# Kernel tuning notes

Measured on AMD Instinct MI355X. Metric: run time of the kernel, lower is better.

The kernel has to match this reference:

```python
import jax, jax.numpy as jnp
import numpy as np

N_NODES = 50000
N_EDGES = 800000
D_IN = 256
H = 4
D_OUT = 64
NEG_SLOPE = 0.2


def setup_inputs() -> dict:
    key = jax.random.key(0)
    ks = jax.random.split(key, 6)
    feat = jax.random.normal(ks[0], (N_NODES, D_IN), dtype=jnp.float32)
    src = jax.random.randint(ks[1], (N_EDGES,), 0, N_NODES, dtype=jnp.int32)
    dst = jax.random.randint(ks[2], (N_EDGES,), 0, N_NODES, dtype=jnp.int32)
    # Glorot-ish scaled params
    W_src = jax.random.normal(ks[3], (H * D_OUT, D_IN), dtype=jnp.float32) * (1.0 / np.sqrt(D_IN))
    W_dst = jax.random.normal(ks[4], (H * D_OUT, D_IN), dtype=jnp.float32) * (1.0 / np.sqrt(D_IN))
    b_src = jnp.zeros((H * D_OUT,), dtype=jnp.float32)
    b_dst = jnp.zeros((H * D_OUT,), dtype=jnp.float32)
    attn = jax.random.normal(ks[5], (H, D_OUT), dtype=jnp.float32) * (1.0 / np.sqrt(D_OUT))
    return {"feat": feat, "src": src, "dst": dst, "W_src": W_src, "b_src": b_src,
            "W_dst": W_dst, "b_dst": b_dst, "attn": attn}


def reference(feat, src, dst, W_src, b_src, W_dst, b_dst, attn):
    n = feat.shape[0]
    h, d = attn.shape
    # node projections [N, H, D]
    feat_src = (feat @ W_src.T + b_src).reshape(n, h, d)
    feat_dst = (feat @ W_dst.T + b_dst).reshape(n, h, d)
    # edge-wise u + v, LeakyReLU  -> [E, H, D]
    e = jax.nn.leaky_relu(feat_src[src] + feat_dst[dst], negative_slope=NEG_SLOPE)
    # attention logits [E, H]
    score = jnp.einsum('ehd,hd->eh', e, attn)
    # edge softmax over incoming edges per dst node (numerically stable)
    m = jax.ops.segment_max(score, dst, num_segments=n)
    expv = jnp.exp(score - m[dst])
    denom = jax.ops.segment_sum(expv, dst, num_segments=n)
    a = expv / denom[dst]  # [E, H]
    # weighted scatter-sum of source features -> [N, H, D]
    out = jax.ops.segment_sum(feat_src[src] * a[:, :, None], dst, num_segments=n)
    return out
```

## Files before the change

kernel.cpp:

```cpp
#include <hip/hip_runtime.h>
#include <math.h>

#define N_DIN 256
#define N_COUT 256
#define NEG_SLOPE 0.2f
#define L2E 1.44269504f
#define CAP 64

#define LDK2 40

typedef _Float16 f16;
typedef f16 f16x2 __attribute__((ext_vector_type(2)));
typedef f16 f16x4 __attribute__((ext_vector_type(4)));
typedef f16 f16x8 __attribute__((ext_vector_type(8)));
typedef float f32x4 __attribute__((ext_vector_type(4)));
typedef float f32x8 __attribute__((ext_vector_type(8)));

__global__ __launch_bounds__(256) void prep2(
    const float* __restrict__ Wsrc, const float* __restrict__ Wdst,
    f16* __restrict__ wsrc_h, f16* __restrict__ wdst_h,
    int* __restrict__ deg, int n)
{
    const int b = blockIdx.x;
    if (b >= 64) {
        int i = (b - 64) * 256 + threadIdx.x;
        if (i < n) deg[i] = 0;
        return;
    }
    const float* __restrict__ in = (b < 32) ? Wsrc : Wdst;
    f16* __restrict__ out        = (b < 32) ? wsrc_h : wdst_h;
    size_t i = (size_t)(b & 31) * 2048 + (size_t)threadIdx.x * 8;
    float4 v0 = *reinterpret_cast<const float4*>(&in[i]);
    float4 v1 = *reinterpret_cast<const float4*>(&in[i + 4]);
    f16x8 o;
    o[0] = (f16)v0.x; o[1] = (f16)v0.y; o[2] = (f16)v0.z; o[3] = (f16)v0.w;
    o[4] = (f16)v1.x; o[5] = (f16)v1.y; o[6] = (f16)v1.z; o[7] = (f16)v1.w;
    *reinterpret_cast<f16x8*>(&out[i]) = o;
}

__global__ __launch_bounds__(512) void projbucket(
    const float* __restrict__ feat,
    const f16* __restrict__ wsrc_h, const float* __restrict__ bsrc,
    const f16* __restrict__ wdst_h, const float* __restrict__ bdst,
    f16* __restrict__ fsrc_h, f16* __restrict__ fdst_h, int n,
    const int* __restrict__ src, const int* __restrict__ dst,
    int* __restrict__ deg, int* __restrict__ ssrc, int E)
{
    __shared__ f16 Al[2][64 * LDK2];

    const int t = threadIdx.x;
    const int bx = (int)blockIdx.x;

    if (bx % 3 != 0) {
        int bid = bx - bx / 3 - 1;
        int i = bid * 512 + t;
        if (i < E) {
            int d = dst[i];
            int r = atomicAdd(&deg[d], 1);
            if (r < CAP) ssrc[(size_t)d * CAP + r] = src[i];
        }
        return;
    }
    const int gid = bx / 3;

    const int lane = t & 63;
    const int w = t >> 6;
    const int which = w >> 2;
    const int col0 = (w & 3) * 64;
    const f16* __restrict__ Wm     = which ? wdst_h : wsrc_h;
    const float* __restrict__ bias = which ? bdst : bsrc;
    f16* __restrict__ outp         = which ? fdst_h : fsrc_h;
    const int row0 = gid * 64;

    const int lr = lane & 15;
    const int kc = lane >> 4;

    const int arow = t >> 3;
    const int akof = (t & 7) * 4;
    int agrow = row0 + arow;
    if (agrow >= n) agrow = n - 1;
    const float* __restrict__ fbase = &feat[(size_t)agrow * N_DIN + akof];
    const f16* __restrict__ wrow[4] = {
        &Wm[(size_t)(col0 + 0 * 16 + lr) * N_DIN + kc * 8],
        &Wm[(size_t)(col0 + 1 * 16 + lr) * N_DIN + kc * 8],
        &Wm[(size_t)(col0 + 2 * 16 + lr) * N_DIN + kc * 8],
        &Wm[(size_t)(col0 + 3 * 16 + lr) * N_DIN + kc * 8] };

    f32x4 acc[4][4] = {};

    {
        float4 u = *reinterpret_cast<const float4*>(fbase);
        f16x4 av;
        av[0] = (f16)u.x; av[1] = (f16)u.y; av[2] = (f16)u.z; av[3] = (f16)u.w;
        *reinterpret_cast<f16x4*>(&Al[0][arow * LDK2 + akof]) = av;
    }
    f16x8 Wcur[4], Wnxt[4];
    #pragma unroll
    for (int nf = 0; nf < 4; ++nf)
        Wcur[nf] = *reinterpret_cast<const f16x8*>(wrow[nf]);
    __syncthreads();

    int p = 0;
    #pragma unroll
    for (int ks = 0; ks < 8; ++ks) {
        const int k0 = ks * 32;
        float4 nx;
        if (ks < 7) {
            nx = *reinterpret_cast<const float4*>(fbase + k0 + 32);
            #pragma unroll
            for (int nf = 0; nf < 4; ++nf)
                Wnxt[nf] = *reinterpret_cast<const f16x8*>(wrow[nf] + k0 + 32);
        }

        f16x8 afr[4];
        #pragma unroll
        for (int m = 0; m < 4; ++m)
            afr[m] = *reinterpret_cast<const f16x8*>(
                &Al[p][(m * 16 + lr) * LDK2 + kc * 8]);
        #pragma unroll
        for (int nf = 0; nf < 4; ++nf)
            #pragma unroll
            for (int m = 0; m < 4; ++m)
                acc[nf][m] = __builtin_amdgcn_mfma_f32_16x16x32_f16(
                    Wcur[nf], afr[m], acc[nf][m], 0, 0, 0);

        if (ks < 7) {
            f16x4 av;
            av[0] = (f16)nx.x; av[1] = (f16)nx.y; av[2] = (f16)nx.z; av[3] = (f16)nx.w;
            *reinterpret_cast<f16x4*>(&Al[p ^ 1][arow * LDK2 + akof]) = av;
            __syncthreads();
            #pragma unroll
            for (int nf = 0; nf < 4; ++nf) Wcur[nf] = Wnxt[nf];
            p ^= 1;
        }
    }

    #pragma unroll
    for (int nf = 0; nf < 4; ++nf) {
        const int cbase = col0 + nf * 16 + kc * 4;
        const float4 bv = *reinterpret_cast<const float4*>(&bias[cbase]);
        #pragma unroll
        for (int m = 0; m < 4; ++m) {
            const int row = row0 + m * 16 + lr;
            if (row < n) {
                f16x4 o;
                o[0] = (f16)(acc[nf][m][0] + bv.x);
                o[1] = (f16)(acc[nf][m][1] + bv.y);
                o[2] = (f16)(acc[nf][m][2] + bv.z);
                o[3] = (f16)(acc[nf][m][3] + bv.w);
                *reinterpret_cast<f16x4*>(&outp[(size_t)row * N_COUT + cbase]) = o;
            }
        }
    }
}


template<int Q>
__device__ __forceinline__ void gat_batch(
    int e0, int i0m, int i1m,
    const f16* __restrict__ fsrc_h, int cb,
    f16x8 fd, f16x8 aw, f16x8 zz, f16x8 slp,
    float& l, f32x8& acc)
{
    f16x8 fr[Q];
    #pragma unroll
    for (int q = 0; q < Q; ++q) {
        int e = e0 + q;
        int u = __shfl((e < 32) ? i0m : i1m, e & 31, 32);
        fr[q] = *reinterpret_cast<const f16x8*>(&fsrc_h[(size_t)u * N_COUT + cb]);
    }
    float s[Q];
    #pragma unroll
    for (int q = 0; q < Q; ++q) {
        f16x8 x = fr[q] + fd;
        f16x8 e = slp * __builtin_elementwise_min(x, zz)
                + __builtin_elementwise_max(x, zz);
        f16x2 e0v = { e[0], e[1] }, e1v = { e[2], e[3] };
        f16x2 e2v = { e[4], e[5] }, e3v = { e[6], e[7] };
        f16x2 a0 = { aw[0], aw[1] }, a1 = { aw[2], aw[3] };
        f16x2 a2 = { aw[4], aw[5] }, a3 = { aw[6], aw[7] };
        s[q] = __builtin_amdgcn_fdot2(e3v, a3,
                __builtin_amdgcn_fdot2(e2v, a2,
                 __builtin_amdgcn_fdot2(e1v, a1,
                  __builtin_amdgcn_fdot2(e0v, a0, 0.f, false), false), false), false);
    }
    #pragma unroll
    for (int o = 1; o < 8; o <<= 1) {
        #pragma unroll
        for (int q = 0; q < Q; ++q) s[q] += __shfl_xor(s[q], o);
    }
    float ls = 0.f;
    #pragma unroll
    for (int q = 0; q < Q; ++q) {
        float p = exp2f(s[q]);
        #pragma unroll
        for (int k = 0; k < 8; ++k)
            acc[k] = fmaf((float)fr[q][k], p, acc[k]);
        ls += p;
    }
    l += ls;
}

__global__ __launch_bounds__(256) void gat16(
    const f16* __restrict__ fsrc_h, const f16* __restrict__ fdst_h,
    const float* __restrict__ attn, const int* __restrict__ deg,
    const int* __restrict__ ssrc, float* __restrict__ out, int n)
{
    const int t = threadIdx.x;
    const int v = blockIdx.x * 8 + (t >> 5);
    if (v >= n) return;
    const int lane = t & 31;
    const int cb = lane * 8;

    float4 aw0 = *reinterpret_cast<const float4*>(&attn[cb]);
    float4 aw1 = *reinterpret_cast<const float4*>(&attn[cb + 4]);
    f16x8 aw;
    aw[0] = (f16)(aw0.x * L2E); aw[1] = (f16)(aw0.y * L2E);
    aw[2] = (f16)(aw0.z * L2E); aw[3] = (f16)(aw0.w * L2E);
    aw[4] = (f16)(aw1.x * L2E); aw[5] = (f16)(aw1.y * L2E);
    aw[6] = (f16)(aw1.z * L2E); aw[7] = (f16)(aw1.w * L2E);
    const f16x8 zz = { (f16)0.f, (f16)0.f, (f16)0.f, (f16)0.f,
                       (f16)0.f, (f16)0.f, (f16)0.f, (f16)0.f };
    const f16x8 slp = { (f16)NEG_SLOPE, (f16)NEG_SLOPE, (f16)NEG_SLOPE, (f16)NEG_SLOPE,
                        (f16)NEG_SLOPE, (f16)NEG_SLOPE, (f16)NEG_SLOPE, (f16)NEG_SLOPE };

    f16x8 fd = *reinterpret_cast<const f16x8*>(&fdst_h[(size_t)v * N_COUT + cb]);

    int cnt = deg[v];
    if (cnt > CAP) cnt = CAP;
    const int base = v * CAP;

    int i0m = ssrc[base + lane];
    int i1m = ssrc[base + 32 + lane];

    float l = 0.f;
    f32x8 acc = {};

    int i = 0;
    for (; i + 8 <= cnt; i += 8)
        gat_batch<8>(i, i0m, i1m, fsrc_h, cb, fd, aw, zz, slp, l, acc);
    if (i + 4 <= cnt) {
        gat_batch<4>(i, i0m, i1m, fsrc_h, cb, fd, aw, zz, slp, l, acc);
        i += 4;
    }
    for (; i < cnt; ++i)
        gat_batch<1>(i, i0m, i1m, fsrc_h, cb, fd, aw, zz, slp, l, acc);

    const float inv = (l > 0.f) ? (1.0f / l) : 0.f;
    #pragma unroll
    for (int k = 0; k < 8; ++k) acc[k] *= inv;
    *reinterpret_cast<f32x8*>(&out[(size_t)v * N_COUT + cb]) = acc;
}

extern "C" void kernel_launch(void* const* d_in, const int* in_sizes, int n_in,
                              void* d_out, int out_size, void* d_ws, size_t ws_size,
                              hipStream_t stream)
{
    const float* feat = (const float*)d_in[0];
    const int*   src  = (const int*)d_in[1];
    const int*   dst  = (const int*)d_in[2];
    const float* Wsrc = (const float*)d_in[3];
    const float* bsrc = (const float*)d_in[4];
    const float* Wdst = (const float*)d_in[5];
    const float* bdst = (const float*)d_in[6];
    const float* attn = (const float*)d_in[7];

    const int N = in_sizes[0] / N_DIN;
    const int E = in_sizes[1];
    float* out = (float*)d_out;

    char* ws = (char*)d_ws;
    f16* wsrc_h = (f16*)ws; ws += (size_t)N_COUT * N_DIN * sizeof(f16);
    f16* wdst_h = (f16*)ws; ws += (size_t)N_COUT * N_DIN * sizeof(f16);
    f16* fsrc_h = (f16*)ws; ws += (size_t)N * N_COUT * sizeof(f16);
    f16* fdst_h = (f16*)ws; ws += (size_t)N * N_COUT * sizeof(f16);
    int* deg    = (int*)ws; ws += (size_t)N * sizeof(int);
    int* ssrc   = (int*)ws; ws += (size_t)N * CAP * sizeof(int);

    const int ngemm = (N + 63) / 64;
    const int nbkt  = (E + 511) / 512;

    prep2<<<64 + (N + 255) / 256, 256, 0, stream>>>(Wsrc, Wdst, wsrc_h, wdst_h, deg, N);

    projbucket<<<ngemm + nbkt, 512, 0, stream>>>(
        feat, wsrc_h, bsrc, wdst_h, bdst, fsrc_h, fdst_h, N,
        src, dst, deg, ssrc, E);

    gat16<<<(N + 7) / 8, 256, 0, stream>>>(fsrc_h, fdst_h, attn, deg, ssrc, out, N);
}
```

Baseline: 140.2 us.

## Stage full A tile in LDS once and coalesce projection output via LDS

Loads the whole 64x256 feature tile into shared memory up front instead of double-buffering 32-wide K slices with a barrier per step, which removes the per-step syncs. The output is now staged through LDS and written as contiguous 16-byte row segments, two passes for the src and dst halves, replacing scattered 8-byte stores. The cost is a larger LDS footprint (about 33KB), which may lower occupancy, and the loss of the earlier overlap between global loads and MFMA work.

```diff
diff --git a/kernel.cpp b/kernel.cpp
--- a/kernel.cpp
+++ b/kernel.cpp
@@ -6,8 +6,7 @@
 #define NEG_SLOPE 0.2f
 #define L2E 1.44269504f
 #define CAP 64
-
-#define LDK2 40
+#define LDA 264
 
 typedef _Float16 f16;
 typedef f16 f16x2 __attribute__((ext_vector_type(2)));
@@ -46,7 +45,7 @@
     const int* __restrict__ src, const int* __restrict__ dst,
     int* __restrict__ deg, int* __restrict__ ssrc, int E)
 {
-    __shared__ f16 Al[2][64 * LDK2];
+    __shared__ f16 Al[64 * LDA];
 
     const int t = threadIdx.x;
     const int bx = (int)blockIdx.x;
@@ -69,17 +68,29 @@
     const int col0 = (w & 3) * 64;
     const f16* __restrict__ Wm     = which ? wdst_h : wsrc_h;
     const float* __restrict__ bias = which ? bdst : bsrc;
-    f16* __restrict__ outp         = which ? fdst_h : fsrc_h;
     const int row0 = gid * 64;
 
     const int lr = lane & 15;
     const int kc = lane >> 4;
 
     const int arow = t >> 3;
-    const int akof = (t & 7) * 4;
+    const int akof = (t & 7) * 32;
     int agrow = row0 + arow;
     if (agrow >= n) agrow = n - 1;
-    const float* __restrict__ fbase = &feat[(size_t)agrow * N_DIN + akof];
+    {
+        const float* __restrict__ fb = &feat[(size_t)agrow * N_DIN + akof];
+        #pragma unroll
+        for (int j = 0; j < 4; ++j) {
+            float4 u0 = *reinterpret_cast<const float4*>(fb + j * 8);
+            float4 u1 = *reinterpret_cast<const float4*>(fb + j * 8 + 4);
+            f16x8 av;
+            av[0] = (f16)u0.x; av[1] = (f16)u0.y; av[2] = (f16)u0.z; av[3] = (f16)u0.w;
+            av[4] = (f16)u1.x; av[5] = (f16)u1.y; av[6] = (f16)u1.z; av[7] = (f16)u1.w;
+            *reinterpret_cast<f16x8*>(&Al[arow * LDA + akof + j * 8]) = av;
+        }
+    }
+    __syncthreads();
+
     const f16* __restrict__ wrow[4] = {
         &Wm[(size_t)(col0 + 0 * 16 + lr) * N_DIN + kc * 8],
         &Wm[(size_t)(col0 + 1 * 16 + lr) * N_DIN + kc * 8],
@@ -88,72 +99,58 @@
 
     f32x4 acc[4][4] = {};
 
-    {
-        float4 u = *reinterpret_cast<const float4*>(fbase);
-        f16x4 av;
-        av[0] = (f16)u.x; av[1] = (f16)u.y; av[2] = (f16)u.z; av[3] = (f16)u.w;
-        *reinterpret_cast<f16x4*>(&Al[0][arow * LDK2 + akof]) = av;
-    }
-    f16x8 Wcur[4], Wnxt[4];
-    #pragma unroll
-    for (int nf = 0; nf < 4; ++nf)
-        Wcur[nf] = *reinterpret_cast<const f16x8*>(wrow[nf]);
-    __syncthreads();
-
-    int p = 0;
     #pragma unroll
     for (int ks = 0; ks < 8; ++ks) {
         const int k0 = ks * 32;
-        float4 nx;
-        if (ks < 7) {
-            nx = *reinterpret_cast<const float4*>(fbase + k0 + 32);
-            #pragma unroll
-            for (int nf = 0; nf < 4; ++nf)
-                Wnxt[nf] = *reinterpret_cast<const f16x8*>(wrow[nf] + k0 + 32);
-        }
-
+        f16x8 Wf[4];
+        #pragma unroll
+        for (int nf = 0; nf < 4; ++nf)
+            Wf[nf] = *reinterpret_cast<const f16x8*>(wrow[nf] + k0);
         f16x8 afr[4];
         #pragma unroll
         for (int m = 0; m < 4; ++m)
             afr[m] = *reinterpret_cast<const f16x8*>(
-                &Al[p][(m * 16 + lr) * LDK2 + kc * 8]);
+                &Al[(m * 16 + lr) * LDA + k0 + kc * 8]);
         #pragma unroll
         for (int nf = 0; nf < 4; ++nf)
             #pragma unroll
             for (int m = 0; m < 4; ++m)
                 acc[nf][m] = __builtin_amdgcn_mfma_f32_16x16x32_f16(
-                    Wcur[nf], afr[m], acc[nf][m], 0, 0, 0);
-
-        if (ks < 7) {
-            f16x4 av;
-            av[0] = (f16)nx.x; av[1] = (f16)nx.y; av[2] = (f16)nx.z; av[3] = (f16)nx.w;
-            *reinterpret_cast<f16x4*>(&Al[p ^ 1][arow * LDK2 + akof]) = av;
-            __syncthreads();
+                    Wf[nf], afr[m], acc[nf][m], 0, 0, 0);
+    }
+
+    const int erow = t >> 3;
+    const int ecof = (t & 7) * 32;
+    #pragma unroll
+    for (int pass = 0; pass < 2; ++pass) {
+        __syncthreads();
+        if (which == pass) {
             #pragma unroll
-            for (int nf = 0; nf < 4; ++nf) Wcur[nf] = Wnxt[nf];
-            p ^= 1;
-        }
-    }
-
-    #pragma unroll
-    for (int nf = 0; nf < 4; ++nf) {
-        const int cbase = col0 + nf * 16 + kc * 4;
-        const float4 bv = *reinterpret_cast<const float4*>(&bias[cbase]);
-        #pragma unroll
-        for (int m = 0; m < 4; ++m) {
-            const int row = row0 + m * 16 + lr;
-            if (row < n) {
-                f16x4 o;
-                o[0] = (f16)(acc[nf][m][0] + bv.x);
-                o[1] = (f16)(acc[nf][m][1] + bv.y);
-                o[2] = (f16)(acc[nf][m][2] + bv.z);
-                o[3] = (f16)(acc[nf][m][3] + bv.w);
-                *reinterpret_cast<f16x4*>(&outp[(size_t)row * N_COUT + cbase]) = o;
+            for (int nf = 0; nf < 4; ++nf) {
+                const int cbase = col0 + nf * 16 + kc * 4;
+                const float4 bv = *reinterpret_cast<const float4*>(&bias[cbase]);
+                #pragma unroll
+                for (int m = 0; m < 4; ++m) {
+                    f16x4 o;
+                    o[0] = (f16)(acc[nf][m][0] + bv.x);
+                    o[1] = (f16)(acc[nf][m][1] + bv.y);
+                    o[2] = (f16)(acc[nf][m][2] + bv.z);
+                    o[3] = (f16)(acc[nf][m][3] + bv.w);
+                    *reinterpret_cast<f16x4*>(&Al[(m * 16 + lr) * LDA + cbase]) = o;
+                }
             }
         }
-    }
-}
-
+        __syncthreads();
+        if (row0 + erow < n) {
+            f16* __restrict__ op = (pass ? fdst_h : fsrc_h)
+                                 + (size_t)(row0 + erow) * N_COUT + ecof;
+            #pragma unroll
+            for (int j = 0; j < 4; ++j)
+                *reinterpret_cast<f16x8*>(op + j * 8) =
+                    *reinterpret_cast<const f16x8*>(&Al[erow * LDA + ecof + j * 8]);
+        }
+    }
+}
 
 template<int Q>
 __device__ __forceinline__ void gat_batch(
```

Measured after the change: 142.7 us. About the same (+1.7%).

## Retile projection GEMM to 128-row tiles with LDS-staged weights per matrix

Applied to the files above, without the earlier changes.

The projection GEMM block now covers 128 node rows by 256 output columns of a single weight matrix (src or dst picked by block parity), instead of 64 rows by both matrices. Weights are staged cooperatively through shared memory rather than each wave loading its own weight fragments from global memory. The goal is better reuse of feature rows and weights per block. In exchange the register double-buffering prefetch is dropped, so each k-step runs load, sync, compute, sync with no overlap. The block-index interleaving with the bucket blocks also changes, because the GEMM block count stays roughly the same.

```diff
diff --git a/kernel.cpp b/kernel.cpp
--- a/kernel.cpp
+++ b/kernel.cpp
@@ -7,7 +7,8 @@
 #define L2E 1.44269504f
 #define CAP 64
 
-#define LDK2 40
+#define BM 128
+#define LDK 40
 
 typedef _Float16 f16;
 typedef f16 f16x2 __attribute__((ext_vector_type(2)));
@@ -46,7 +47,8 @@
     const int* __restrict__ src, const int* __restrict__ dst,
     int* __restrict__ deg, int* __restrict__ ssrc, int E)
 {
-    __shared__ f16 Al[2][64 * LDK2];
+    __shared__ f16 Al[BM * LDK];
+    __shared__ f16 Bl[256 * LDK];
 
     const int t = threadIdx.x;
     const int bx = (int)blockIdx.x;
@@ -65,83 +67,71 @@
 
     const int lane = t & 63;
     const int w = t >> 6;
-    const int which = w >> 2;
-    const int col0 = (w & 3) * 64;
+    const int wr = w >> 2, wc = w & 3;
+    const int which = gid & 1;
     const f16* __restrict__ Wm     = which ? wdst_h : wsrc_h;
     const float* __restrict__ bias = which ? bdst : bsrc;
     f16* __restrict__ outp         = which ? fdst_h : fsrc_h;
-    const int row0 = gid * 64;
+    const int row0 = (gid >> 1) * BM;
 
     const int lr = lane & 15;
     const int kc = lane >> 4;
 
-    const int arow = t >> 3;
-    const int akof = (t & 7) * 4;
+    const int arow = t >> 2;
+    const int akof = (t & 3) * 8;
+    const int bcol = t >> 1;
+    const int bkof = (t & 1) * 16;
     int agrow = row0 + arow;
     if (agrow >= n) agrow = n - 1;
-    const float* __restrict__ fbase = &feat[(size_t)agrow * N_DIN + akof];
-    const f16* __restrict__ wrow[4] = {
-        &Wm[(size_t)(col0 + 0 * 16 + lr) * N_DIN + kc * 8],
-        &Wm[(size_t)(col0 + 1 * 16 + lr) * N_DIN + kc * 8],
-        &Wm[(size_t)(col0 + 2 * 16 + lr) * N_DIN + kc * 8],
-        &Wm[(size_t)(col0 + 3 * 16 + lr) * N_DIN + kc * 8] };
+    const float* __restrict__ fbase = &feat[(size_t)agrow * N_DIN];
+    const f16* __restrict__ wbase = &Wm[(size_t)bcol * N_DIN];
 
     f32x4 acc[4][4] = {};
 
-    {
-        float4 u = *reinterpret_cast<const float4*>(fbase);
-        f16x4 av;
-        av[0] = (f16)u.x; av[1] = (f16)u.y; av[2] = (f16)u.z; av[3] = (f16)u.w;
-        *reinterpret_cast<f16x4*>(&Al[0][arow * LDK2 + akof]) = av;
-    }
-    f16x8 Wcur[4], Wnxt[4];
-    #pragma unroll
-    for (int nf = 0; nf < 4; ++nf)
-        Wcur[nf] = *reinterpret_cast<const f16x8*>(wrow[nf]);
-    __syncthreads();
-
-    int p = 0;
-    #pragma unroll
-    for (int ks = 0; ks < 8; ++ks) {
-        const int k0 = ks * 32;
-        float4 nx;
-        if (ks < 7) {
-            nx = *reinterpret_cast<const float4*>(fbase + k0 + 32);
-            #pragma unroll
-            for (int nf = 0; nf < 4; ++nf)
-                Wnxt[nf] = *reinterpret_cast<const f16x8*>(wrow[nf] + k0 + 32);
-        }
-
-        f16x8 afr[4];
+    for (int k0 = 0; k0 < N_DIN; k0 += 32) {
+        {
+            const float* fp = fbase + k0 + akof;
+            float4 u0 = *reinterpret_cast<const float4*>(fp);
+            float4 u1 = *reinterpret_cast<const float4*>(fp + 4);
+            f16x8 av;
+            av[0] = (f16)u0.x; av[1] = (f16)u0.y; av[2] = (f16)u0.z; av[3] = (f16)u0.w;
+            av[4] = (f16)u1.x; av[5] = (f16)u1.y; av[6] = (f16)u1.z; av[7] = (f16)u1.w;
+            *reinterpret_cast<f16x8*>(&Al[arow * LDK + akof]) = av;
+        }
+        {
+            const f16* wp = wbase + k0 + bkof;
+            f16x8 v0 = *reinterpret_cast<const f16x8*>(wp);
+            f16x8 v1 = *reinterpret_cast<const f16x8*>(wp + 8);
+            *reinterpret_cast<f16x8*>(&Bl[bcol * LDK + bkof]) = v0;
+            *reinterpret_cast<f16x8*>(&Bl[bcol * LDK + bkof + 8]) = v1;
+        }
+        __syncthreads();
+
+        f16x8 a[4], b[4];
+        #pragma unroll
+        for (int nf = 0; nf < 4; ++nf)
+            a[nf] = *reinterpret_cast<const f16x8*>(
+                &Bl[(wc * 64 + nf * 16 + lr) * LDK + kc * 8]);
         #pragma unroll
         for (int m = 0; m < 4; ++m)
-            afr[m] = *reinterpret_cast<const f16x8*>(
-                &Al[p][(m * 16 + lr) * LDK2 + kc * 8]);
+            b[m] = *reinterpret_cast<const f16x8*>(
+                &Al[(wr * 64 + m * 16 + lr) * LDK + kc * 8]);
         #pragma unroll
         for (int nf = 0; nf < 4; ++nf)
             #pragma unroll
             for (int m = 0; m < 4; ++m)
                 acc[nf][m] = __builtin_amdgcn_mfma_f32_16x16x32_f16(
-                    Wcur[nf], afr[m], acc[nf][m], 0, 0, 0);
-
-        if (ks < 7) {
-            f16x4 av;
-            av[0] = (f16)nx.x; av[1] = (f16)nx.y; av[2] = (f16)nx.z; av[3] = (f16)nx.w;
-            *reinterpret_cast<f16x4*>(&Al[p ^ 1][arow * LDK2 + akof]) = av;
-            __syncthreads();
-            #pragma unroll
-            for (int nf = 0; nf < 4; ++nf) Wcur[nf] = Wnxt[nf];
-            p ^= 1;
-        }
+                    a[nf], b[m], acc[nf][m], 0, 0, 0);
+        __syncthreads();
     }
 
     #pragma unroll
     for (int nf = 0; nf < 4; ++nf) {
-        const int cbase = col0 + nf * 16 + kc * 4;
+        const int cbase = wc * 64 + nf * 16 + kc * 4;
         const float4 bv = *reinterpret_cast<const float4*>(&bias[cbase]);
         #pragma unroll
         for (int m = 0; m < 4; ++m) {
-            const int row = row0 + m * 16 + lr;
+            const int row = row0 + wr * 64 + m * 16 + lr;
             if (row < n) {
                 f16x4 o;
                 o[0] = (f16)(acc[nf][m][0] + bv.x);
@@ -153,7 +143,6 @@
         }
     }
 }
-
 
 template<int Q>
 __device__ __forceinline__ void gat_batch(
@@ -277,7 +266,7 @@
     int* deg    = (int*)ws; ws += (size_t)N * sizeof(int);
     int* ssrc   = (int*)ws; ws += (size_t)N * CAP * sizeof(int);
 
-    const int ngemm = (N + 63) / 64;
+    const int ngemm = 2 * ((N + BM - 1) / BM);
     const int nbkt  = (E + 511) / 512;
 
     prep2<<<64 + (N + 255) / 256, 256, 0, stream>>>(Wsrc, Wdst, wsrc_h, wdst_h, deg, N);
```

Result: no change. 140.3 us (+0.0%).
